# Kernel tuning notes

Measured on AMD Instinct MI355X. Metric: run time of the kernel, lower is better.

The kernel has to match this reference:

```python
import jax, jax.numpy as jnp
import numpy as np

B, S, D = 4, 2048, 2048   # batch, seq, embed
E, R = 64, 64             # experts, expert_rank
INIT_SCALE = 0.02


def setup_inputs() -> dict:
    key = jax.random.key(0)
    k_x, k_m, k_up, k_dn = jax.random.split(key, 4)
    x = jax.random.normal(k_x, (B, S, D), dtype=jnp.float32)
    expert_mask = jax.random.uniform(k_m, (B, S, E), dtype=jnp.float32)
    # up_proj weight, out_first=True: [experts, rank, embed]
    w_up = jax.random.normal(k_up, (E, R, D), dtype=jnp.float32) * INIT_SCALE
    # down_proj weight, out_first=True: [embed, experts, rank]
    w_down = jax.random.normal(k_dn, (D, E, R), dtype=jnp.float32) * INIT_SCALE
    return {"x": x, "expert_mask": expert_mask, "w_up": w_up, "w_down": w_down}


def reference(x, expert_mask, w_up, w_down):
    # up projection: [B,S,D] x [E,R,D] -> [B,S,E,R]
    h = jnp.einsum("bsd,erd->bser", x, w_up)
    h = jax.nn.silu(h)
    # mask inactive experts (broadcast over rank)
    h = h * expert_mask[:, :, :, None]
    # down projection: [B,S,E,R] x [D,E,R] -> [B,S,D]
    out = jnp.einsum("bser,der->bsd", h, w_down)
    return out
```

## Files before the change

### kernel.cpp

```cpp
#include <hip/hip_runtime.h>
#include <hip/hip_bf16.h>

typedef unsigned short u16;
typedef unsigned int   u32;
typedef __attribute__((ext_vector_type(8))) short  s16x8;
typedef __attribute__((ext_vector_type(4))) float  f32x4;
typedef __attribute__((ext_vector_type(4))) unsigned short u16x4;

#define MT    8192
#define DE    2048
#define NEXP  64
#define ERDIM 4096

__device__ __forceinline__ u16 to_bf16(float f) {
  u32 u = __builtin_bit_cast(u32, f);
  u32 r = u + 0x7fffu + ((u >> 16) & 1u);
  return (u16)(r >> 16);
}

__global__ void cvt_f32_bf16(const float* __restrict__ in, u16* __restrict__ out, int n) {
  const int stride = gridDim.x * blockDim.x;
  for (int i = blockIdx.x * blockDim.x + threadIdx.x; i * 4 < n; i += stride) {
    const float4 v = *reinterpret_cast<const float4*>(in + (size_t)i * 4);
    u16x4 o;
    o.x = to_bf16(v.x); o.y = to_bf16(v.y); o.z = to_bf16(v.z); o.w = to_bf16(v.w);
    *reinterpret_cast<u16x4*>(out + (size_t)i * 4) = o;
  }
}

#define GLDS(gp, lp) __builtin_amdgcn_global_load_lds(                        \
    (const __attribute__((address_space(1))) void*)(gp),                      \
    (__attribute__((address_space(3))) void*)(lp), 16, 0, 0)

#define BAR() do { asm volatile("" ::: "memory");                             \
                   __builtin_amdgcn_s_barrier();                              \
                   asm volatile("" ::: "memory"); } while (0)

template<int FUSE, int K>
__global__ __launch_bounds__(512, 2) void gemm_bt(
    const u16* __restrict__ A, const u16* __restrict__ Bm,
    const float* __restrict__ mask, void* __restrict__ Cout,
    const int M, const int N)
{
  constexpr int BM = 256, BN = 256, BK = 32;
  constexpr int NT = K / BK;
  __shared__ __align__(16) u16 lds[65536];

  const int nbn = N / BN;
  const int nwg = (int)gridDim.x;
  const int cpx = nwg >> 3;
  const int bid = (int)blockIdx.x;
  const int swz = (bid & 7) * cpx + (bid >> 3);
  const int bm = (swz / nbn) * BM;
  const int bn = (swz % nbn) * BN;

  const int tid  = (int)threadIdx.x;
  const int lane = tid & 63;
  const int w    = tid >> 6;
  const int wr   = w >> 2;
  const int wc   = w & 3;

  const int fr = lane & 15;
  const int cp = (lane >> 4) ^ ((lane >> 1) & 3);

  const int lr = lane >> 2;
  const int cl = (lane & 3) ^ ((lane >> 3) & 3);
  const int c0 = 2 * w, c1 = 2 * w + 1;
  const u16* aS0 = A  + (size_t)(bm + c0 * 16 + lr) * K + cl * 8;
  const u16* aS1 = A  + (size_t)(bm + c1 * 16 + lr) * K + cl * 8;
  const u16* bS0 = Bm + (size_t)(bn + c0 * 16 + lr) * K + cl * 8;
  const u16* bS1 = Bm + (size_t)(bn + c1 * 16 + lr) * K + cl * 8;

  f32x4 acc[8][4] = {};

#pragma unroll
  for (int t = 0; t < 3; ++t) {
    u16* dst = lds + t * 16384;
    GLDS(aS0 + t * BK, dst +        c0 * 512);
    GLDS(aS1 + t * BK, dst +        c1 * 512);
    GLDS(bS0 + t * BK, dst + 8192 + c0 * 512);
    GLDS(bS1 + t * BK, dst + 8192 + c1 * 512);
  }
  asm volatile("s_waitcnt vmcnt(8)" ::: "memory");
  BAR();

#pragma unroll 4
  for (int t = 0; t < NT; ++t) {
    const u16* sA = lds + (t & 3) * 16384;
    const u16* sB = lds + (t & 3) * 16384 + 8192;
    u16* dst = lds + ((t + 3) & 3) * 16384;
    const bool st = (t + 3 < NT);
    const size_t koff = (size_t)(t + 3) * BK;

    s16x8 a0[4], bfr[4];
#pragma unroll
    for (int m = 0; m < 4; ++m)
      a0[m] = *reinterpret_cast<const s16x8*>(
          &sA[(wr * 128 + m * 16 + fr) * 32 + cp * 8]);
#pragma unroll
    for (int n = 0; n < 4; ++n)
      bfr[n] = *reinterpret_cast<const s16x8*>(
          &sB[(wc * 64 + n * 16 + fr) * 32 + cp * 8]);
    if (st) {
      GLDS(aS0 + koff, dst +        c0 * 512);
      GLDS(aS1 + koff, dst +        c1 * 512);
    }
    BAR();
    __builtin_amdgcn_sched_barrier(0);
    __builtin_amdgcn_s_setprio(1);
#pragma unroll
    for (int m = 0; m < 4; ++m)
#pragma unroll
      for (int n = 0; n < 4; ++n)
        acc[m][n] = __builtin_amdgcn_mfma_f32_16x16x32_bf16(
            a0[m], bfr[n], acc[m][n], 0, 0, 0);
    __builtin_amdgcn_s_setprio(0);
    BAR();

    s16x8 a1[4];
#pragma unroll
    for (int m = 0; m < 4; ++m)
      a1[m] = *reinterpret_cast<const s16x8*>(
          &sA[(wr * 128 + (4 + m) * 16 + fr) * 32 + cp * 8]);
    if (st) {
      GLDS(bS0 + koff, dst + 8192 + c0 * 512);
      GLDS(bS1 + koff, dst + 8192 + c1 * 512);
    }
    if (t + 3 < NT)      asm volatile("s_waitcnt vmcnt(8)" ::: "memory");
    else if (t + 2 < NT) asm volatile("s_waitcnt vmcnt(4)" ::: "memory");
    else if (t + 1 < NT) asm volatile("s_waitcnt vmcnt(0)" ::: "memory");
    BAR();
    __builtin_amdgcn_sched_barrier(0);
    __builtin_amdgcn_s_setprio(1);
#pragma unroll
    for (int m = 0; m < 4; ++m)
#pragma unroll
      for (int n = 0; n < 4; ++n)
        acc[4 + m][n] = __builtin_amdgcn_mfma_f32_16x16x32_bf16(
            a1[m], bfr[n], acc[4 + m][n], 0, 0, 0);
    __builtin_amdgcn_s_setprio(0);
    if (t + 1 < NT) BAR();
  }

  const int rgrp = (lane >> 4) * 4;
  if (FUSE) {
    u16* H = (u16*)Cout;
    const int ew = (bn + wc * 64) >> 6;
#pragma unroll
    for (int m = 0; m < 8; ++m) {
#pragma unroll
      for (int j = 0; j < 4; ++j) {
        const int grow = bm + wr * 128 + m * 16 + rgrp + j;
        const float mv = mask[(size_t)grow * NEXP + ew];
#pragma unroll
        for (int n = 0; n < 4; ++n) {
          const int gcol = bn + wc * 64 + n * 16 + fr;
          float v = acc[m][n][j];
          v = v / (1.0f + __expf(-v));
          H[(size_t)grow * N + gcol] = to_bf16(v * mv);
        }
      }
    }
  } else {
    float* O = (float*)Cout;
#pragma unroll
    for (int m = 0; m < 8; ++m) {
#pragma unroll
      for (int j = 0; j < 4; ++j) {
        const int grow = bm + wr * 128 + m * 16 + rgrp + j;
#pragma unroll
        for (int n = 0; n < 4; ++n) {
          const int gcol = bn + wc * 64 + n * 16 + fr;
          O[(size_t)grow * N + gcol] = acc[m][n][j];
        }
      }
    }
  }
}

extern "C" void kernel_launch(void* const* d_in, const int* in_sizes, int n_in,
                              void* d_out, int out_size, void* d_ws, size_t ws_size,
                              hipStream_t stream) {
  const float* x     = (const float*)d_in[0];
  const float* emask = (const float*)d_in[1];
  const float* w_up  = (const float*)d_in[2];
  const float* w_dn  = (const float*)d_in[3];
  float* out = (float*)d_out;

  const size_t need = ((size_t)MT * DE + (size_t)ERDIM * DE + (size_t)DE * ERDIM +
                       (size_t)MT * ERDIM) * sizeof(u16);
  if (ws_size < need) return;

  u16* xb  = (u16*)d_ws;
  u16* wub = xb  + (size_t)MT * DE;
  u16* wdb = wub + (size_t)ERDIM * DE;
  u16* hb  = wdb + (size_t)DE * ERDIM;

  hipLaunchKernelGGL(cvt_f32_bf16, dim3(2048), dim3(256), 0, stream, x,    xb,  MT * DE);
  hipLaunchKernelGGL(cvt_f32_bf16, dim3(1024), dim3(256), 0, stream, w_up, wub, ERDIM * DE);
  hipLaunchKernelGGL(cvt_f32_bf16, dim3(1024), dim3(256), 0, stream, w_dn, wdb, DE * ERDIM);

  hipLaunchKernelGGL((gemm_bt<1, DE>), dim3((MT / 256) * (ERDIM / 256)), dim3(512), 0, stream,
                     xb, wub, emask, (void*)hb, MT, ERDIM);
  hipLaunchKernelGGL((gemm_bt<0, ERDIM>), dim3((MT / 256) * (DE / 256)), dim3(512), 0, stream,
                     hb, wdb, nullptr, (void*)out, MT, DE);
}
```

Baseline: 291.7 us.

## Software-pipeline GEMM main loop with register double-buffered B fragments

Restructures the K loop so the second half-tile MFMAs of step t-1 run while the A/B fragments of step t are read from LDS. B fragments alternate between two register sets. All four global-to-LDS loads are issued together, and each K step now has one barrier instead of three. The aim is to cut barrier stalls and hide LDS read latency behind MFMA work, at the cost of more live registers under the 512-thread, 2-block launch bound and more complex prologue and epilogue handling.

New measurement: 290.3 us. About the same (-0.5%).

```diff
diff --git a/kernel.cpp b/kernel.cpp
--- a/kernel.cpp
+++ b/kernel.cpp
@@ -84,63 +84,103 @@
   asm volatile("s_waitcnt vmcnt(8)" ::: "memory");
   BAR();
 
-#pragma unroll 4
-  for (int t = 0; t < NT; ++t) {
-    const u16* sA = lds + (t & 3) * 16384;
-    const u16* sB = lds + (t & 3) * 16384 + 8192;
-    u16* dst = lds + ((t + 3) & 3) * 16384;
-    const bool st = (t + 3 < NT);
-    const size_t koff = (size_t)(t + 3) * BK;
-
-    s16x8 a0[4], bfr[4];
+  s16x8 a0[4], a1[4], b0[4], b1[4];
+
+  {
+    const u16* sA = lds;
+    const u16* sB = lds + 8192;
 #pragma unroll
     for (int m = 0; m < 4; ++m)
       a0[m] = *reinterpret_cast<const s16x8*>(
           &sA[(wr * 128 + m * 16 + fr) * 32 + cp * 8]);
 #pragma unroll
     for (int n = 0; n < 4; ++n)
-      bfr[n] = *reinterpret_cast<const s16x8*>(
+      b0[n] = *reinterpret_cast<const s16x8*>(
           &sB[(wc * 64 + n * 16 + fr) * 32 + cp * 8]);
-    if (st) {
-      GLDS(aS0 + koff, dst +        c0 * 512);
-      GLDS(aS1 + koff, dst +        c1 * 512);
-    }
-    BAR();
-    __builtin_amdgcn_sched_barrier(0);
-    __builtin_amdgcn_s_setprio(1);
-#pragma unroll
-    for (int m = 0; m < 4; ++m)
-#pragma unroll
-      for (int n = 0; n < 4; ++n)
-        acc[m][n] = __builtin_amdgcn_mfma_f32_16x16x32_bf16(
-            a0[m], bfr[n], acc[m][n], 0, 0, 0);
-    __builtin_amdgcn_s_setprio(0);
-    BAR();
-
-    s16x8 a1[4];
 #pragma unroll
     for (int m = 0; m < 4; ++m)
       a1[m] = *reinterpret_cast<const s16x8*>(
           &sA[(wr * 128 + (4 + m) * 16 + fr) * 32 + cp * 8]);
-    if (st) {
-      GLDS(bS0 + koff, dst + 8192 + c0 * 512);
-      GLDS(bS1 + koff, dst + 8192 + c1 * 512);
-    }
-    if (t + 3 < NT)      asm volatile("s_waitcnt vmcnt(8)" ::: "memory");
-    else if (t + 2 < NT) asm volatile("s_waitcnt vmcnt(4)" ::: "memory");
-    else if (t + 1 < NT) asm volatile("s_waitcnt vmcnt(0)" ::: "memory");
+    u16* dst = lds + 3 * 16384;
+    GLDS(aS0 + 3 * BK, dst +        c0 * 512);
+    GLDS(aS1 + 3 * BK, dst +        c1 * 512);
+    GLDS(bS0 + 3 * BK, dst + 8192 + c0 * 512);
+    GLDS(bS1 + 3 * BK, dst + 8192 + c1 * 512);
+    __builtin_amdgcn_s_setprio(1);
+#pragma unroll
+    for (int m = 0; m < 4; ++m)
+#pragma unroll
+      for (int n = 0; n < 4; ++n)
+        acc[m][n] = __builtin_amdgcn_mfma_f32_16x16x32_bf16(
+            a0[m], b0[n], acc[m][n], 0, 0, 0);
+    __builtin_amdgcn_s_setprio(0);
+    asm volatile("s_waitcnt vmcnt(8)" ::: "memory");
     BAR();
-    __builtin_amdgcn_sched_barrier(0);
-    __builtin_amdgcn_s_setprio(1);
-#pragma unroll
-    for (int m = 0; m < 4; ++m)
-#pragma unroll
-      for (int n = 0; n < 4; ++n)
-        acc[4 + m][n] = __builtin_amdgcn_mfma_f32_16x16x32_bf16(
-            a1[m], bfr[n], acc[4 + m][n], 0, 0, 0);
-    __builtin_amdgcn_s_setprio(0);
-    if (t + 1 < NT) BAR();
-  }
+  }
+
+#define BODY(T, BIN, BOUT, LAST)                                              \
+  {                                                                           \
+    const u16* sA = lds + ((T) & 3) * 16384;                                  \
+    const u16* sB = sA + 8192;                                                \
+    _Pragma("unroll")                                                         \
+    for (int m = 0; m < 4; ++m)                                               \
+      a0[m] = *reinterpret_cast<const s16x8*>(                                \
+          &sA[(wr * 128 + m * 16 + fr) * 32 + cp * 8]);                       \
+    _Pragma("unroll")                                                         \
+    for (int n = 0; n < 4; ++n)                                               \
+      BOUT[n] = *reinterpret_cast<const s16x8*>(                              \
+          &sB[(wc * 64 + n * 16 + fr) * 32 + cp * 8]);                        \
+    if ((T) + 3 < NT) {                                                       \
+      u16* dst = lds + (((T) + 3) & 3) * 16384;                               \
+      const size_t koff = (size_t)((T) + 3) * BK;                             \
+      GLDS(aS0 + koff, dst +        c0 * 512);                                \
+      GLDS(aS1 + koff, dst +        c1 * 512);                                \
+      GLDS(bS0 + koff, dst + 8192 + c0 * 512);                                \
+      GLDS(bS1 + koff, dst + 8192 + c1 * 512);                                \
+    }                                                                         \
+    __builtin_amdgcn_s_setprio(1);                                            \
+    _Pragma("unroll")                                                         \
+    for (int m = 0; m < 4; ++m)                                               \
+      _Pragma("unroll")                                                       \
+      for (int n = 0; n < 4; ++n)                                             \
+        acc[4 + m][n] = __builtin_amdgcn_mfma_f32_16x16x32_bf16(              \
+            a1[m], BIN[n], acc[4 + m][n], 0, 0, 0);                           \
+    __builtin_amdgcn_s_setprio(0);                                            \
+    _Pragma("unroll")                                                         \
+    for (int m = 0; m < 4; ++m)                                               \
+      a1[m] = *reinterpret_cast<const s16x8*>(                                \
+          &sA[(wr * 128 + (4 + m) * 16 + fr) * 32 + cp * 8]);                 \
+    __builtin_amdgcn_s_setprio(1);                                            \
+    _Pragma("unroll")                                                         \
+    for (int m = 0; m < 4; ++m)                                               \
+      _Pragma("unroll")                                                       \
+      for (int n = 0; n < 4; ++n)                                             \
+        acc[m][n] = __builtin_amdgcn_mfma_f32_16x16x32_bf16(                  \
+            a0[m], BOUT[n], acc[m][n], 0, 0, 0);                              \
+    __builtin_amdgcn_s_setprio(0);                                            \
+    if (!(LAST)) {                                                            \
+      if ((T) + 3 < NT)      asm volatile("s_waitcnt vmcnt(8)" ::: "memory"); \
+      else if ((T) + 2 < NT) asm volatile("s_waitcnt vmcnt(4)" ::: "memory"); \
+      else if ((T) + 1 < NT) asm volatile("s_waitcnt vmcnt(0)" ::: "memory"); \
+      BAR();                                                                  \
+    }                                                                         \
+  }
+
+  for (int tt = 1; tt + 2 < NT; tt += 2) {
+    BODY(tt,     b0, b1, false);
+    BODY(tt + 1, b1, b0, false);
+  }
+  BODY(NT - 1, b0, b1, true);
+#undef BODY
+
+  __builtin_amdgcn_s_setprio(1);
+#pragma unroll
+  for (int m = 0; m < 4; ++m)
+#pragma unroll
+    for (int n = 0; n < 4; ++n)
+      acc[4 + m][n] = __builtin_amdgcn_mfma_f32_16x16x32_bf16(
+          a1[m], b1[n], acc[4 + m][n], 0, 0, 0);
+  __builtin_amdgcn_s_setprio(0);
 
   const int rgrp = (lane >> 4) * 4;
   if (FUSE) {
```
